# Kernel tuning notes

Hardware: AMD Instinct MI355X
Metric: run time of the kernel (lower is better)

Reference implementation:

```python
import jax, jax.numpy as jnp
import numpy as np

B, S, H = 8, 1024, 1024
NH, HD = 16, 64  # num heads, head dim


def _split_heads(x):
    # [B,S,H] -> [B,NH,S,HD]
    return x.reshape(B, S, NH, HD).transpose(0, 2, 1, 3)


def setup_inputs() -> dict:
    key = jax.random.key(0)
    ks = jax.random.split(key, 16)
    sc = 1.0 / np.sqrt(H)
    sch = 1.0 / np.sqrt(HD)
    return {
        "hidden_states": jax.random.normal(ks[0], (B, S, H), jnp.float32),
        "attention_mask": jnp.zeros((B, 1, 1, S), jnp.float32),
        "context_embedded": jax.random.normal(ks[1], (B, S, H), jnp.float32),
        "Wq": jax.random.normal(ks[2], (H, H), jnp.float32) * sc,
        "bq": jnp.zeros((H,), jnp.float32),
        "Wk": jax.random.normal(ks[3], (H, H), jnp.float32) * sc,
        "bk": jnp.zeros((H,), jnp.float32),
        "Wv": jax.random.normal(ks[4], (H, H), jnp.float32) * sc,
        "bv": jnp.zeros((H,), jnp.float32),
        "Wcq": jax.random.normal(ks[5], (HD, HD), jnp.float32) * sch,
        "bcq": jnp.zeros((HD,), jnp.float32),
        "Wck": jax.random.normal(ks[6], (HD, HD), jnp.float32) * sch,
        "bck": jnp.zeros((HD,), jnp.float32),
        "w_lqc": jax.random.normal(ks[7], (HD,), jnp.float32) * sch,
        "w_lqq": jax.random.normal(ks[8], (HD,), jnp.float32) * sch,
        "w_lkc": jax.random.normal(ks[9], (HD,), jnp.float32) * sch,
        "w_lkk": jax.random.normal(ks[10], (HD,), jnp.float32) * sch,
    }


def reference(hidden_states, attention_mask, context_embedded,
              Wq, bq, Wk, bk, Wv, bv, Wcq, bcq, Wck, bck,
              w_lqc, w_lqq, w_lkc, w_lkk):
    # projections -> [B,NH,S,HD]
    q = _split_heads(hidden_states @ Wq + bq)
    k = _split_heads(hidden_states @ Wk + bk)
    v = _split_heads(hidden_states @ Wv + bv)
    ce = _split_heads(context_embedded)

    # context gating for queries
    ce_q = ce @ Wcq + bcq
    lam_q = jax.nn.sigmoid(ce_q @ w_lqc[:, None] + q @ w_lqq[:, None])  # [B,NH,S,1]
    q_ctx = (1.0 - lam_q) * q + lam_q * ce_q

    # context gating for keys
    ce_k = ce @ Wck + bck
    lam_k = jax.nn.sigmoid(ce_k @ w_lkc[:, None] + k @ w_lkk[:, None])  # [B,NH,S,1]
    k_ctx = (1.0 - lam_k) * k + lam_k * ce_k

    scores = jnp.einsum("bhqd,bhkd->bhqk", q_ctx, k_ctx) / np.sqrt(HD)
    scores = scores + attention_mask
    probs = jax.nn.softmax(scores, axis=-1)
    ctx = jnp.einsum("bhqk,bhkd->bhqd", probs, v)
    return ctx.transpose(0, 2, 1, 3).reshape(B, S, H)
```

## Files before the change

### kernel.cpp

```cpp
#include <hip/hip_runtime.h>

typedef _Float16 f16;
typedef f16   f16x8 __attribute__((ext_vector_type(8)));
typedef float f32x4 __attribute__((ext_vector_type(4)));

namespace {
constexpr int kB  = 8;
constexpr int kS  = 1024;
constexpr int kH  = 1024;
constexpr int kNH = 16;
constexpr int kHD = 64;
constexpr int kBH = kB * kNH;
constexpr int kRows = kBH * kS;
}

__device__ __forceinline__ void async16(const f16* g, f16* l) {
    __builtin_amdgcn_global_load_lds(
        (const __attribute__((address_space(1))) unsigned int*)g,
        (__attribute__((address_space(3))) unsigned int*)l, 16, 0, 0);
}

__device__ __forceinline__ int phys4(int m, int c) {
    return ((m >> 1) << 3) | ((((m & 1) << 2) | c) ^ ((m >> 1) & 7));
}
__device__ __forceinline__ int phys8(int m, int c) {
    return (m << 3) | (c ^ (m & 7));
}

__global__ __launch_bounds__(256) void cast_inputs_kernel(
    const float* __restrict__ hs, const float* __restrict__ ce,
    f16* __restrict__ hs16, f16* __restrict__ ce16)
{
    int i = (blockIdx.x * 256 + threadIdx.x) * 8;
    const float* src = blockIdx.y ? ce : hs;
    float4 a = *(const float4*)(src + i);
    float4 b = *(const float4*)(src + i + 4);
    union { f16 h[8]; uint4 u; } pk;
    pk.h[0] = (f16)a.x; pk.h[1] = (f16)a.y; pk.h[2] = (f16)a.z; pk.h[3] = (f16)a.w;
    pk.h[4] = (f16)b.x; pk.h[5] = (f16)b.y; pk.h[6] = (f16)b.z; pk.h[7] = (f16)b.w;
    if (blockIdx.y == 0) {
        *(uint4*)(hs16 + i) = pk.u;
    } else {
        int row = i >> 10, col = i & 1023;
        int bb = row >> 10, s = row & 1023;
        int h = col >> 6, d = col & 63;
        size_t o = ((((size_t)(bb * kNH + h) << 10) | s) << 6) | d;
        *(uint4*)(ce16 + o) = pk.u;
    }
}

__global__ __launch_bounds__(256) void transpose_w_kernel(
    const float* __restrict__ Wq, const float* __restrict__ Wk,
    const float* __restrict__ Wv, f16* __restrict__ Wt)
{
    const float* W = (blockIdx.z == 0) ? Wq : (blockIdx.z == 1) ? Wk : Wv;
    f16* out = Wt + (size_t)blockIdx.z * kH * kH;
    __shared__ f16 T[64][72];
    const int tid = threadIdx.x;
    const int k0 = blockIdx.y * 64, n0 = blockIdx.x * 64;
#pragma unroll
    for (int i = 0; i < 4; ++i) {
        int idx = tid + i * 256;
        int r = idx >> 4, cb = (idx & 15) * 4;
        float4 v = *(const float4*)(W + (size_t)(k0 + r) * kH + n0 + cb);
        T[cb + 0][r] = (f16)v.x; T[cb + 1][r] = (f16)v.y;
        T[cb + 2][r] = (f16)v.z; T[cb + 3][r] = (f16)v.w;
    }
    __syncthreads();
#pragma unroll
    for (int i = 0; i < 4; ++i) {
        int idx = tid + i * 256;
        int r = idx >> 4, cb = (idx & 15) * 4;
        union { f16 h[4]; uint2 u; } pk;
#pragma unroll
        for (int j = 0; j < 4; ++j) pk.h[j] = T[r][cb + j];
        *(uint2*)(out + (size_t)(n0 + r) * kH + k0 + cb) = pk.u;
    }
}

__global__ __launch_bounds__(256) void prep_small_kernel(
    const float* __restrict__ Wcq, const float* __restrict__ Wck,
    const float* __restrict__ mask,
    f16* __restrict__ Wct, unsigned int* __restrict__ kn,
    float* __restrict__ mm)
{
    const int t = threadIdx.x;
    if (blockIdx.x < 2) {
        const float* W = blockIdx.x ? Wck : Wcq;
        f16* out = Wct + blockIdx.x * kHD * kHD;
#pragma unroll
        for (int i = 0; i < 16; ++i) {
            int idx = i * 256 + t;
            int k = idx >> 6, n = idx & 63;
            out[n * 64 + k] = (f16)W[idx];
        }
        if (blockIdx.x == 0 && t < kBH) kn[t] = 0u;
    } else {
        const int b = blockIdx.x - 2;
        const float* mp = mask + b * kS;
        float v = fmaxf(fmaxf(mp[t], mp[t + 256]), fmaxf(mp[t + 512], mp[t + 768]));
#pragma unroll
        for (int off = 1; off < 64; off <<= 1) v = fmaxf(v, __shfl_xor(v, off, 64));
        __shared__ float red[4];
        if ((t & 63) == 0) red[t >> 6] = v;
        __syncthreads();
        if (t == 0) mm[b] = fmaxf(fmaxf(red[0], red[1]), fmaxf(red[2], red[3]));
    }
}

__global__ __launch_bounds__(256) void qkv_gemm_f16(
    const f16* __restrict__ hs16, const f16* __restrict__ Wt,
    const float* __restrict__ bq, const float* __restrict__ bk,
    const float* __restrict__ bv,
    f16* __restrict__ q16, f16* __restrict__ k16, f16* __restrict__ vt)
{
    const int z = blockIdx.z;
    const f16* Bmat = Wt + (size_t)z * kH * kH;
    const float* bias = (z == 0) ? bq : (z == 1) ? bk : bv;

    __shared__ f16 AB[2][2][128 * 32];

    const int tid = threadIdx.x;
    const int w = tid >> 6, lane = tid & 63;
    const int quad = lane >> 4, mh = lane & 15;
    const int wm = w >> 1, wn = w & 1;
    const int m0 = blockIdx.x * 128, n0 = blockIdx.y * 128;

    const f16* aptr[2]; const f16* bptr[2];
#pragma unroll
    for (int i = 0; i < 2; ++i) {
        int P = (w * 2 + i) * 64 + lane;
        int r2 = P >> 3, s = P & 7;
        int bb = s ^ (r2 & 7);
        int m = (r2 << 1) | (bb >> 2), c = bb & 3;
        aptr[i] = hs16 + (size_t)(m0 + m) * kH + c * 8;
        bptr[i] = Bmat + (size_t)(n0 + m) * kH + c * 8;
    }

    auto issue = [&](int buf) {
#pragma unroll
        for (int i = 0; i < 2; ++i) {
            async16(aptr[i], AB[buf][0] + (w * 2 + i) * 512);
            async16(bptr[i], AB[buf][1] + (w * 2 + i) * 512);
            aptr[i] += 32; bptr[i] += 32;
        }
    };

    f32x4 acc[4][4];
#pragma unroll
    for (int i = 0; i < 4; ++i)
#pragma unroll
        for (int j = 0; j < 4; ++j) acc[i][j] = (f32x4){0.f, 0.f, 0.f, 0.f};

    int aoff[4], boff[4];
#pragma unroll
    for (int t = 0; t < 4; ++t) {
        aoff[t] = phys4(wm * 64 + t * 16 + mh, quad) * 8;
        boff[t] = phys4(wn * 64 + t * 16 + mh, quad) * 8;
    }

    auto compute = [&](int buf) {
        f16x8 af[4], bf[4];
#pragma unroll
        for (int t = 0; t < 4; ++t) af[t] = *(const f16x8*)(AB[buf][0] + aoff[t]);
#pragma unroll
        for (int t = 0; t < 4; ++t) bf[t] = *(const f16x8*)(AB[buf][1] + boff[t]);
#pragma unroll
        for (int i = 0; i < 4; ++i)
#pragma unroll
            for (int j = 0; j < 4; ++j)
                acc[i][j] = __builtin_amdgcn_mfma_f32_16x16x32_f16(
                    af[i], bf[j], acc[i][j], 0, 0, 0);
    };

    issue(0);
    __syncthreads();

    for (int it = 0; it < 16; ++it) {
        issue(1);
        compute(0);
        __syncthreads();
        if (it < 15) issue(0);
        compute(1);
        __syncthreads();
    }

    if (z < 2) {
        f16* outp = (z == 0) ? q16 : k16;
        f16* Cb = &AB[0][0][0] + w * 1280;
        const int h    = (n0 + wn * 64) >> 6;
        const int bbb  = m0 >> 10;
        const int sb   = (m0 & 1023) + wm * 64;
        f16* base = outp + ((size_t)(bbb * kNH + h) * kS + sb) * kHD;
#pragma unroll
        for (int nt = 0; nt < 4; ++nt) {
            const float bn = bias[n0 + wn * 64 + nt * 16 + mh];
#pragma unroll
            for (int mt = 0; mt < 4; ++mt)
#pragma unroll
                for (int r = 0; r < 4; ++r)
                    Cb[(mt * 16 + quad * 4 + r) * 20 + mh] =
                        (f16)(acc[mt][nt][r] + bn);
#pragma unroll
            for (int p = 0; p < 4; ++p) {
                int row = (lane >> 2) + p * 16;
                int qtr = lane & 3;
                uint2 v = *(const uint2*)(&Cb[row * 20 + qtr * 4]);
                *(uint2*)(base + (size_t)row * kHD + nt * 16 + qtr * 4) = v;
            }
        }
    } else {
#pragma unroll
        for (int nt = 0; nt < 4; ++nt) {
            const int n = n0 + wn * 64 + nt * 16 + mh;
            const int h = n >> 6, d = n & 63;
            const float bn = bias[n];
#pragma unroll
            for (int mt = 0; mt < 4; ++mt) {
                int mbase = m0 + wm * 64 + mt * 16 + quad * 4;
                int bbb = mbase >> 10, s0 = mbase & 1023;
                union { f16 h4[4]; uint2 u; } pk;
#pragma unroll
                for (int r = 0; r < 4; ++r) pk.h4[r] = (f16)(acc[mt][nt][r] + bn);
                *(uint2*)(vt + ((size_t)(bbb * kNH + h) * kHD + d) * kS + s0) = pk.u;
            }
        }
    }
}

__global__ __launch_bounds__(256) void gate_mfma(
    const f16* __restrict__ ce16, const f16* __restrict__ Wct,
    const float* __restrict__ bcq, const float* __restrict__ bck,
    const float* __restrict__ wlqc, const float* __restrict__ wlqq,
    const float* __restrict__ wlkc, const float* __restrict__ wlkk,
    f16* __restrict__ q16, f16* __restrict__ k16,
    unsigned int* __restrict__ kn)
{
    __shared__ f16 Wls[64 * 64];
    __shared__ f16 CeQ[4][64 * 64];
    __shared__ float Tp[4][64 * 17];
    __shared__ float lamS[4][64];

    const int tid = threadIdx.x, w = tid >> 6, lane = tid & 63;
    const int quad = lane >> 4, mh = lane & 15;
    const int gate = blockIdx.x >> 9;
    const int tIdx = (blockIdx.x & 511) * 4 + w;
    const size_t row0 = (size_t)tIdx * 64;

    const float* bc  = gate ? bck  : bcq;
    const float* wlc = gate ? wlkc : wlqc;
    const float* wlx = gate ? wlkk : wlqq;
    f16* xw = (gate ? k16 : q16) + row0 * kHD;
    const f16* cep = ce16 + row0 * kHD;
    const f16* Wcg = Wct + gate * kHD * kHD;

#pragma unroll
    for (int i = 0; i < 2; ++i) {
        int P = tid + i * 256;
        int m = P >> 3, c = P & 7;
        *(uint4*)(Wls + phys8(m, c) * 8) = *(const uint4*)(Wcg + m * 64 + c * 8);
    }
#pragma unroll
    for (int i = 0; i < 8; ++i) {
        int P = i * 64 + lane;
        int m = P >> 3, c = (P & 7) ^ (m & 7);
        async16(cep + m * 64 + c * 8, CeQ[w] + i * 512);
    }
    __syncthreads();

#pragma unroll
    for (int it = 0; it < 8; ++it) {
        int slot = it * 64 + lane;
        int r = slot >> 3, c = slot & 7;
        union { uint4 u; f16 h[8]; } xv;
        xv.u = *(const uint4*)(xw + r * 64 + c * 8);
        float4 wa = ((const float4*)wlx)[c * 2];
        float4 wb = ((const float4*)wlx)[c * 2 + 1];
        float s = (float)xv.h[0] * wa.x + (float)xv.h[1] * wa.y +
                  (float)xv.h[2] * wa.z + (float)xv.h[3] * wa.w +
                  (float)xv.h[4] * wb.x + (float)xv.h[5] * wb.y +
                  (float)xv.h[6] * wb.z + (float)xv.h[7] * wb.w;
        s += __shfl_xor(s, 1, 64);
        s += __shfl_xor(s, 2, 64);
        s += __shfl_xor(s, 4, 64);
        if ((lane & 7) == 0) Tp[w][r * 17 + 16] = s;
    }

    f32x4 acc[4][4];
#pragma unroll
    for (int i = 0; i < 4; ++i)
#pragma unroll
        for (int j = 0; j < 4; ++j) acc[i][j] = (f32x4){0.f, 0.f, 0.f, 0.f};

    f16x8 bfr[4][2];
#pragma unroll
    for (int nt = 0; nt < 4; ++nt)
#pragma unroll
        for (int ks = 0; ks < 2; ++ks)
            bfr[nt][ks] = *(const f16x8*)(Wls + phys8(nt * 16 + mh, ks * 4 + quad) * 8);
#pragma unroll
    for (int mt = 0; mt < 4; ++mt) {
        f16x8 a0 = *(const f16x8*)(CeQ[w] + phys8(mt * 16 + mh, 0 + quad) * 8);
        f16x8 a1 = *(const f16x8*)(CeQ[w] + phys8(mt * 16 + mh, 4 + quad) * 8);
#pragma unroll
        for (int nt = 0; nt < 4; ++nt) {
            acc[mt][nt] = __builtin_amdgcn_mfma_f32_16x16x32_f16(a0, bfr[nt][0], acc[mt][nt], 0, 0, 0);
            acc[mt][nt] = __builtin_amdgcn_mfma_f32_16x16x32_f16(a1, bfr[nt][1], acc[mt][nt], 0, 0, 0);
        }
    }

    float bcv[4], wlcv[4];
#pragma unroll
    for (int nt = 0; nt < 4; ++nt) {
        int n = nt * 16 + mh;
        bcv[nt] = bc[n]; wlcv[nt] = wlc[n];
    }
#pragma unroll
    for (int mt = 0; mt < 4; ++mt) {
#pragma unroll
        for (int r = 0; r < 4; ++r) {
            int m = mt * 16 + quad * 4 + r;
            float tpv = 0.f;
#pragma unroll
            for (int nt = 0; nt < 4; ++nt) {
                float v = acc[mt][nt][r] + bcv[nt];
                int col = nt * 16 + mh;
                CeQ[w][phys8(m, col >> 3) * 8 + (col & 7)] = (f16)v;
                tpv += v * wlcv[nt];
            }
            Tp[w][m * 17 + mh] = tpv;
        }
    }

    float t = 0.f;
#pragma unroll
    for (int j = 0; j < 17; ++j) t += Tp[w][lane * 17 + j];
    lamS[w][lane] = 1.0f / (1.0f + __expf(-t));

    float wmax = 0.f;
#pragma unroll
    for (int it = 0; it < 8; ++it) {
        int slot = it * 64 + lane;
        int r = slot >> 3, c = slot & 7;
        float lam = lamS[w][r];
        union { uint4 u; f16 h[8]; } xv;
        xv.u = *(const uint4*)(xw + r * 64 + c * 8);
        f16x8 cq = *(const f16x8*)(CeQ[w] + phys8(r, c) * 8);
        union { f16 h[8]; uint4 u; } o;
        float ss = 0.f;
#pragma unroll
        for (int j = 0; j < 8; ++j) {
            o.h[j] = (f16)((1.0f - lam) * (float)xv.h[j] + lam * (float)cq[j]);
            float fv = (float)o.h[j];
            ss += fv * fv;
        }
        *(uint4*)(xw + r * 64 + c * 8) = o.u;
        if (gate) {
            ss += __shfl_xor(ss, 1, 64);
            ss += __shfl_xor(ss, 2, 64);
            ss += __shfl_xor(ss, 4, 64);
            wmax = fmaxf(wmax, ss);
        }
    }
    if (gate) {
        wmax = fmaxf(wmax, __shfl_xor(wmax, 8, 64));
        wmax = fmaxf(wmax, __shfl_xor(wmax, 16, 64));
        wmax = fmaxf(wmax, __shfl_xor(wmax, 32, 64));
        if (lane == 0) atomicMax(&kn[tIdx >> 4], __float_as_uint(wmax));
    }
}

__global__ __launch_bounds__(256) void attn_f16(
    const f16* __restrict__ q16, const f16* __restrict__ k16,
    const f16* __restrict__ vt, const float* __restrict__ mask,
    const unsigned int* __restrict__ kn, const float* __restrict__ mm,
    float* __restrict__ out)
{
    __shared__ f16 Ks[2][64 * 64];
    __shared__ f16 Vs[2][64 * 64];
    __shared__ f16 Ps[4][32 * 68];

    const int tid = threadIdx.x;
    const int w = tid >> 6, lane = tid & 63;
    const int quad = lane >> 4, mh = lane & 15;
    const int bh = blockIdx.x, bbb = bh >> 4, h = bh & 15;
    const int q0 = blockIdx.y * 128;
    const float* maskb = mask + bbb * kS;

    int mS[2], cS[2];
#pragma unroll
    for (int i = 0; i < 2; ++i) {
        int P = (w * 2 + i) * 64 + lane;
        mS[i] = P >> 3;
        cS[i] = (P & 7) ^ (mS[i] & 7);
    }
    const f16* kp[2]; const f16* vp[2];
#pragma unroll
    for (int i = 0; i < 2; ++i) {
        kp[i] = k16 + ((size_t)bh * kS + mS[i]) * kHD + cS[i] * 8;
        vp[i] = vt  + ((size_t)bh * kHD + mS[i]) * kS + cS[i] * 8;
    }

    auto issue = [&](f16* Kb, f16* Vb) {
#pragma unroll
        for (int i = 0; i < 2; ++i) {
            async16(kp[i], Kb + (w * 2 + i) * 512);
            async16(vp[i], Vb + (w * 2 + i) * 512);
            kp[i] += 64 * kHD;
            vp[i] += 64;
        }
    };

    issue(Ks[0], Vs[0]);

    f16x8 qf[2][2];
#pragma unroll
    for (int rt = 0; rt < 2; ++rt) {
        const f16* qrow = q16 + ((size_t)bh * kS + q0 + w * 32 + rt * 16 + mh) * kHD;
#pragma unroll
        for (int ks = 0; ks < 2; ++ks) {
            qf[rt][ks] = *(const f16x8*)(qrow + ks * 32 + quad * 8);
#pragma unroll
            for (int j = 0; j < 8; ++j) qf[rt][ks][j] *= (f16)0.125f;
        }
    }

    const float kn2 = __uint_as_float(kn[bh]);
    const float mmb = mm[bbb];
    float bndr[2][4];
#pragma unroll
    for (int rt = 0; rt < 2; ++rt) {
        float qn2 = 0.f;
#pragma unroll
        for (int ks = 0; ks < 2; ++ks)
#pragma unroll
            for (int j = 0; j < 8; ++j) {
                float v = (float)qf[rt][ks][j];
                qn2 += v * v;
            }
        qn2 += __shfl_xor(qn2, 16, 64);
        qn2 += __shfl_xor(qn2, 32, 64);
        const float bnd = sqrtf(qn2 * kn2) + mmb - 9.5f;
#pragma unroll
        for (int r = 0; r < 4; ++r) bndr[rt][r] = __shfl(bnd, quad * 4 + r, 64);
    }

    f32x4 O[2][4];
#pragma unroll
    for (int rt = 0; rt < 2; ++rt)
#pragma unroll
        for (int i = 0; i < 4; ++i) O[rt][i] = (f32x4){0.f, 0.f, 0.f, 0.f};
    float lsum[2][4] = {{0.f, 0.f, 0.f, 0.f}, {0.f, 0.f, 0.f, 0.f}};

    auto step = [&](const f16* Kb, const f16* Vb, int jt) {
        f32x4 S[2][4];
#pragma unroll
        for (int nt = 0; nt < 4; ++nt) {
            f16x8 kf0 = *(const f16x8*)(Kb + phys8(nt * 16 + mh, 0 + quad) * 8);
            f16x8 kf1 = *(const f16x8*)(Kb + phys8(nt * 16 + mh, 4 + quad) * 8);
#pragma unroll
            for (int rt = 0; rt < 2; ++rt) {
                S[rt][nt] = __builtin_amdgcn_mfma_f32_16x16x32_f16(
                    qf[rt][0], kf0, (f32x4){0.f, 0.f, 0.f, 0.f}, 0, 0, 0);
                S[rt][nt] = __builtin_amdgcn_mfma_f32_16x16x32_f16(
                    qf[rt][1], kf1, S[rt][nt], 0, 0, 0);
            }
        }
#pragma unroll
        for (int nt = 0; nt < 4; ++nt) {
            const float mv = maskb[jt + nt * 16 + mh];
#pragma unroll
            for (int rt = 0; rt < 2; ++rt)
#pragma unroll
                for (int r = 0; r < 4; ++r) {
                    float e = __expf(S[rt][nt][r] + mv - bndr[rt][r]);
                    lsum[rt][r] += e;
                    Ps[w][(rt * 16 + quad * 4 + r) * 68 + nt * 16 + mh] = (f16)e;
                }
        }
        f16x8 pf[2][2];
#pragma unroll
        for (int rt = 0; rt < 2; ++rt)
#pragma unroll
            for (int ks = 0; ks < 2; ++ks)
                pf[rt][ks] = *(const f16x8*)(
                    &Ps[w][(rt * 16 + mh) * 68 + ks * 32 + quad * 8]);
#pragma unroll
        for (int dt = 0; dt < 4; ++dt) {
            f16x8 vf0 = *(const f16x8*)(Vb + phys8(dt * 16 + mh, 0 + quad) * 8);
            f16x8 vf1 = *(const f16x8*)(Vb + phys8(dt * 16 + mh, 4 + quad) * 8);
#pragma unroll
            for (int rt = 0; rt < 2; ++rt) {
                O[rt][dt] = __builtin_amdgcn_mfma_f32_16x16x32_f16(
                    pf[rt][0], vf0, O[rt][dt], 0, 0, 0);
                O[rt][dt] = __builtin_amdgcn_mfma_f32_16x16x32_f16(
                    pf[rt][1], vf1, O[rt][dt], 0, 0, 0);
            }
        }
    };

    __syncthreads();

    for (int jt = 0; jt < kS; jt += 128) {
        issue(Ks[1], Vs[1]);
        step(Ks[0], Vs[0], jt);
        __syncthreads();
        if (jt + 128 < kS) issue(Ks[0], Vs[0]);
        step(Ks[1], Vs[1], jt + 64);
        __syncthreads();
    }

#pragma unroll
    for (int rt = 0; rt < 2; ++rt)
#pragma unroll
        for (int r = 0; r < 4; ++r) {
#pragma unroll
            for (int off = 1; off < 16; off <<= 1)
                lsum[rt][r] += __shfl_xor(lsum[rt][r], off, 64);
            lsum[rt][r] = 1.0f / lsum[rt][r];
        }
#pragma unroll
    for (int rt = 0; rt < 2; ++rt)
#pragma unroll
        for (int dt = 0; dt < 4; ++dt)
#pragma unroll
            for (int r = 0; r < 4; ++r) {
                const int s = q0 + w * 32 + rt * 16 + quad * 4 + r;
                out[((size_t)(bbb * kS + s)) * kH + (h << 6) + dt * 16 + mh] =
                    O[rt][dt][r] * lsum[rt][r];
            }
}

extern "C" void kernel_launch(void* const* d_in, const int* in_sizes, int n_in,
                              void* d_out, int out_size, void* d_ws, size_t ws_size,
                              hipStream_t stream) {
    (void)in_sizes; (void)n_in; (void)out_size; (void)ws_size;

    const float* hs   = (const float*)d_in[0];
    const float* mask = (const float*)d_in[1];
    const float* ce   = (const float*)d_in[2];
    const float* Wq   = (const float*)d_in[3];
    const float* bq   = (const float*)d_in[4];
    const float* Wk   = (const float*)d_in[5];
    const float* bk   = (const float*)d_in[6];
    const float* Wv   = (const float*)d_in[7];
    const float* bv   = (const float*)d_in[8];
    const float* Wcq  = (const float*)d_in[9];
    const float* bcq  = (const float*)d_in[10];
    const float* Wck  = (const float*)d_in[11];
    const float* bck  = (const float*)d_in[12];
    const float* wlqc = (const float*)d_in[13];
    const float* wlqq = (const float*)d_in[14];
    const float* wlkc = (const float*)d_in[15];
    const float* wlkk = (const float*)d_in[16];
    float* out = (float*)d_out;

    f16* hs16 = (f16*)d_ws;
    f16* Wt   = hs16 + (size_t)kB * kS * kH;
    f16* q16  = Wt + (size_t)3 * kH * kH;
    f16* k16  = q16 + (size_t)kRows * kHD;
    f16* vt   = k16 + (size_t)kRows * kHD;
    f16* ce16 = vt + (size_t)kRows * kHD;
    f16* Wct  = ce16 + (size_t)kRows * kHD;
    unsigned int* kn = (unsigned int*)(Wct + 2 * kHD * kHD);
    float* mm = (float*)(kn + kBH);

    cast_inputs_kernel<<<dim3(kB * kS * kH / (256 * 8), 2), 256, 0, stream>>>(
        hs, ce, hs16, ce16);
    transpose_w_kernel<<<dim3(16, 16, 3), 256, 0, stream>>>(Wq, Wk, Wv, Wt);
    prep_small_kernel<<<dim3(10), 256, 0, stream>>>(Wcq, Wck, mask, Wct, kn, mm);

    qkv_gemm_f16<<<dim3(kB * kS / 128, kH / 128, 3), 256, 0, stream>>>(
        hs16, Wt, bq, bk, bv, q16, k16, vt);

    gate_mfma<<<dim3(1024), 256, 0, stream>>>(
        ce16, Wct, bcq, bck, wlqc, wlqq, wlkc, wlkk, q16, k16, kn);

    attn_f16<<<dim3(kBH, kS / 128), 256, 0, stream>>>(
        q16, k16, vt, mask, kn, mm, out);
}
```

Measured before the change: 323.7 us.

## Transpose PV MFMA with ds_read_tr P staging, per-row-tile loop, vector stores

Restructures the attention step so each 16-row tile computes QK^T, exponentiates, and packs P into a small per-wave transposed LDS buffer. P is then read back with ds_read_b64_tr_b16, and the PV product is computed as V^T·P^T so the output accumulator is laid out per query row. The epilogue redistributes row sums via shuffles and writes 16-byte nontemporal vector stores instead of scalar stores. It also adds setprio hints around MFMA blocks and a min-blocks launch bound. The goals are lower LDS footprint and traffic for P, fewer scalar global stores, and better overlap, at the cost of inline asm with explicit waitcnts that may serialize the LDS reads.

```diff
diff --git a/kernel.cpp b/kernel.cpp
--- a/kernel.cpp
+++ b/kernel.cpp
@@ -2,6 +2,7 @@
 
 typedef _Float16 f16;
 typedef f16   f16x8 __attribute__((ext_vector_type(8)));
+typedef f16   f16x4 __attribute__((ext_vector_type(4)));
 typedef float f32x4 __attribute__((ext_vector_type(4)));
 
 namespace {
@@ -370,7 +371,7 @@
     }
 }
 
-__global__ __launch_bounds__(256) void attn_f16(
+__global__ __launch_bounds__(256, 4) void attn_f16(
     const f16* __restrict__ q16, const f16* __restrict__ k16,
     const f16* __restrict__ vt, const float* __restrict__ mask,
     const unsigned int* __restrict__ kn, const float* __restrict__ mm,
@@ -378,7 +379,7 @@
 {
     __shared__ f16 Ks[2][64 * 64];
     __shared__ f16 Vs[2][64 * 64];
-    __shared__ f16 Ps[4][32 * 68];
+    __shared__ f16 Pt[4][64 * 16];
 
     const int tid = threadIdx.x;
     const int w = tid >> 6, lane = tid & 63;
@@ -413,6 +414,10 @@
 
     issue(Ks[0], Vs[0]);
 
+    f16* PtW = &Pt[w][0];
+    const __attribute__((address_space(3))) f16* ptr_tr =
+        (const __attribute__((address_space(3))) f16*)PtW + quad * 128 + mh * 4;
+
     f16x8 qf[2][2];
 #pragma unroll
     for (int rt = 0; rt < 2; ++rt) {
@@ -453,49 +458,62 @@
     float lsum[2][4] = {{0.f, 0.f, 0.f, 0.f}, {0.f, 0.f, 0.f, 0.f}};
 
     auto step = [&](const f16* Kb, const f16* Vb, int jt) {
-        f32x4 S[2][4];
-#pragma unroll
-        for (int nt = 0; nt < 4; ++nt) {
-            f16x8 kf0 = *(const f16x8*)(Kb + phys8(nt * 16 + mh, 0 + quad) * 8);
-            f16x8 kf1 = *(const f16x8*)(Kb + phys8(nt * 16 + mh, 4 + quad) * 8);
-#pragma unroll
-            for (int rt = 0; rt < 2; ++rt) {
-                S[rt][nt] = __builtin_amdgcn_mfma_f32_16x16x32_f16(
+        float mv[4];
+#pragma unroll
+        for (int nt = 0; nt < 4; ++nt) mv[nt] = maskb[jt + nt * 16 + mh];
+#pragma unroll
+        for (int rt = 0; rt < 2; ++rt) {
+            f32x4 S[4];
+            __builtin_amdgcn_s_setprio(1);
+#pragma unroll
+            for (int nt = 0; nt < 4; ++nt) {
+                f16x8 kf0 = *(const f16x8*)(Kb + phys8(nt * 16 + mh, 0 + quad) * 8);
+                f16x8 kf1 = *(const f16x8*)(Kb + phys8(nt * 16 + mh, 4 + quad) * 8);
+                S[nt] = __builtin_amdgcn_mfma_f32_16x16x32_f16(
                     qf[rt][0], kf0, (f32x4){0.f, 0.f, 0.f, 0.f}, 0, 0, 0);
-                S[rt][nt] = __builtin_amdgcn_mfma_f32_16x16x32_f16(
-                    qf[rt][1], kf1, S[rt][nt], 0, 0, 0);
-            }
-        }
-#pragma unroll
-        for (int nt = 0; nt < 4; ++nt) {
-            const float mv = maskb[jt + nt * 16 + mh];
-#pragma unroll
-            for (int rt = 0; rt < 2; ++rt)
+                S[nt] = __builtin_amdgcn_mfma_f32_16x16x32_f16(
+                    qf[rt][1], kf1, S[nt], 0, 0, 0);
+            }
+            __builtin_amdgcn_s_setprio(0);
+#pragma unroll
+            for (int nt = 0; nt < 4; ++nt) {
+                union { f16 h4[4]; uint2 u; } pk;
 #pragma unroll
                 for (int r = 0; r < 4; ++r) {
-                    float e = __expf(S[rt][nt][r] + mv - bndr[rt][r]);
+                    float e = __expf(S[nt][r] + mv[nt] - bndr[rt][r]);
                     lsum[rt][r] += e;
-                    Ps[w][(rt * 16 + quad * 4 + r) * 68 + nt * 16 + mh] = (f16)e;
+                    pk.h4[r] = (f16)e;
                 }
-        }
-        f16x8 pf[2][2];
-#pragma unroll
-        for (int rt = 0; rt < 2; ++rt)
-#pragma unroll
-            for (int ks = 0; ks < 2; ++ks)
-                pf[rt][ks] = *(const f16x8*)(
-                    &Ps[w][(rt * 16 + mh) * 68 + ks * 32 + quad * 8]);
-#pragma unroll
-        for (int dt = 0; dt < 4; ++dt) {
-            f16x8 vf0 = *(const f16x8*)(Vb + phys8(dt * 16 + mh, 0 + quad) * 8);
-            f16x8 vf1 = *(const f16x8*)(Vb + phys8(dt * 16 + mh, 4 + quad) * 8);
-#pragma unroll
-            for (int rt = 0; rt < 2; ++rt) {
+                *(uint2*)(PtW + (nt * 16 + mh) * 16 + quad * 4) = pk.u;
+            }
+            f16x8 vf[4][2];
+#pragma unroll
+            for (int dt = 0; dt < 4; ++dt) {
+                vf[dt][0] = *(const f16x8*)(Vb + phys8(dt * 16 + mh, 0 + quad) * 8);
+                vf[dt][1] = *(const f16x8*)(Vb + phys8(dt * 16 + mh, 4 + quad) * 8);
+            }
+            f16x4 t0, t1, t2, t3;
+            asm volatile(
+                "s_waitcnt lgkmcnt(0)\n\t"
+                "ds_read_b64_tr_b16 %0, %4\n\t"
+                "ds_read_b64_tr_b16 %1, %4 offset:128\n\t"
+                "ds_read_b64_tr_b16 %2, %4 offset:1024\n\t"
+                "ds_read_b64_tr_b16 %3, %4 offset:1152\n\t"
+                "s_waitcnt lgkmcnt(0)"
+                : "=&v"(t0), "=&v"(t1), "=&v"(t2), "=&v"(t3)
+                : "v"(ptr_tr) : "memory");
+            __builtin_amdgcn_sched_barrier(0);
+            f16x8 p0 = __builtin_shufflevector(t0, t1, 0, 1, 2, 3, 4, 5, 6, 7);
+            f16x8 p1 = __builtin_shufflevector(t2, t3, 0, 1, 2, 3, 4, 5, 6, 7);
+            __builtin_amdgcn_s_setprio(1);
+#pragma unroll
+            for (int dt = 0; dt < 4; ++dt) {
                 O[rt][dt] = __builtin_amdgcn_mfma_f32_16x16x32_f16(
-                    pf[rt][0], vf0, O[rt][dt], 0, 0, 0);
+                    vf[dt][0], p0, O[rt][dt], 0, 0, 0);
                 O[rt][dt] = __builtin_amdgcn_mfma_f32_16x16x32_f16(
-                    pf[rt][1], vf1, O[rt][dt], 0, 0, 0);
-            }
+                    vf[dt][1], p1, O[rt][dt], 0, 0, 0);
+            }
+            __builtin_amdgcn_s_setprio(0);
         }
     };
 
@@ -517,18 +535,33 @@
 #pragma unroll
             for (int off = 1; off < 16; off <<= 1)
                 lsum[rt][r] += __shfl_xor(lsum[rt][r], off, 64);
-            lsum[rt][r] = 1.0f / lsum[rt][r];
-        }
-#pragma unroll
-    for (int rt = 0; rt < 2; ++rt)
-#pragma unroll
-        for (int dt = 0; dt < 4; ++dt)
-#pragma unroll
-            for (int r = 0; r < 4; ++r) {
-                const int s = q0 + w * 32 + rt * 16 + quad * 4 + r;
-                out[((size_t)(bbb * kS + s)) * kH + (h << 6) + dt * 16 + mh] =
-                    O[rt][dt][r] * lsum[rt][r];
-            }
+        }
+    const int srcl = ((mh >> 2) << 4) + mh;
+    float inv[2];
+#pragma unroll
+    for (int rt = 0; rt < 2; ++rt) {
+        float l0 = __shfl(lsum[rt][0], srcl, 64);
+        float l1 = __shfl(lsum[rt][1], srcl, 64);
+        float l2 = __shfl(lsum[rt][2], srcl, 64);
+        float l3 = __shfl(lsum[rt][3], srcl, 64);
+        float a = (mh & 1) ? l1 : l0;
+        float b = (mh & 1) ? l3 : l2;
+        inv[rt] = 1.0f / ((mh & 2) ? b : a);
+    }
+#pragma unroll
+    for (int rt = 0; rt < 2; ++rt) {
+        const int s = q0 + w * 32 + rt * 16 + mh;
+        float* orow = out + ((size_t)(bbb * kS + s)) * kH + (h << 6);
+#pragma unroll
+        for (int dt = 0; dt < 4; ++dt) {
+            f32x4 v;
+            v[0] = O[rt][dt][0] * inv[rt];
+            v[1] = O[rt][dt][1] * inv[rt];
+            v[2] = O[rt][dt][2] * inv[rt];
+            v[3] = O[rt][dt][3] * inv[rt];
+            __builtin_nontemporal_store(v, (f32x4*)(orow + dt * 16 + quad * 4));
+        }
+    }
 }
 
 extern "C" void kernel_launch(void* const* d_in, const int* in_sizes, int n_in,
```

Measured after the change: 431.2 us. 33.2% more time.
